# Performance work log

Measured on AMD Instinct MI355X. Metric: run time of the kernel, lower is better.

Reference implementation:

```python
import jax, jax.numpy as jnp
import numpy as np

DIM = 3456      # visual_dim
E = 1024        # embed_dim = dim_head*heads = 128*8
H = 8
D = E // H
LN_EPS = 1e-5


def _mlp(x, w1, b1, w2, b2):
    # nn.Sequential(Linear, GELU(exact), Linear)
    h = jax.nn.gelu(x @ w1.T + b1, approximate=False)
    return h @ w2.T + b2


def _ln(x, g, b):
    m = jnp.mean(x, axis=-1, keepdims=True)
    v = jnp.mean((x - m) ** 2, axis=-1, keepdims=True)
    return (x - m) * jax.lax.rsqrt(v + LN_EPS) * g + b


def setup_inputs() -> dict:
    key = jax.random.key(0)
    ks = jax.random.split(key, 24)
    std = 0.02
    d = {"x": jax.random.normal(ks[0], (5, 729, DIM), dtype=jnp.float32)}
    i = 1
    for name in ("q", "k", "v"):
        d[f"{name}_w1"] = std * jax.random.normal(ks[i], (E, DIM), dtype=jnp.float32); i += 1
        d[f"{name}_b1"] = jnp.zeros((E,), jnp.float32)
        d[f"{name}_w2"] = std * jax.random.normal(ks[i], (E, E), dtype=jnp.float32); i += 1
        d[f"{name}_b2"] = jnp.zeros((E,), jnp.float32)
        d[f"ln_{name}_g"] = jnp.ones((E,), jnp.float32)
        d[f"ln_{name}_b"] = jnp.zeros((E,), jnp.float32)
    d["in_proj_w"] = std * jax.random.normal(ks[i], (3 * E, E), dtype=jnp.float32); i += 1
    d["in_proj_b"] = jnp.zeros((3 * E,), jnp.float32)
    d["out_proj_w"] = std * jax.random.normal(ks[i], (E, E), dtype=jnp.float32); i += 1
    d["out_proj_b"] = jnp.zeros((E,), jnp.float32)
    d["to_out_w"] = std * jax.random.normal(ks[i], (DIM, E), dtype=jnp.float32)
    return d


def reference(x,
              q_w1, q_b1, q_w2, q_b2, ln_q_g, ln_q_b,
              k_w1, k_b1, k_w2, k_b2, ln_k_g, ln_k_b,
              v_w1, v_b1, v_w2, v_b2, ln_v_g, ln_v_b,
              in_proj_w, in_proj_b, out_proj_w, out_proj_b, to_out_w):
    t, hw, c = x.shape
    # spatial_temporal pattern: x_multi = x, no interpolation.
    # q/k/v: MLP -> LN -> permute(1,0,2) -> divide_feature -> flatten.
    # divide_feature is a pure permutation of tokens; all tokens end up in a
    # single (L, 1, E) attention, so full attention over the flattened
    # (hw, t) token order computes the identical result.
    q = _ln(_mlp(x, q_w1, q_b1, q_w2, q_b2), ln_q_g, ln_q_b)  # (t, hw, E)
    k = _ln(_mlp(x, k_w1, k_b1, k_w2, k_b2), ln_k_g, ln_k_b)
    v = _ln(_mlp(x, v_w1, v_b1, v_w2, v_b2), ln_v_g, ln_v_b)
    L = t * hw
    q = q.transpose(1, 0, 2).reshape(L, E)  # (hw*t, E), (h,w,t)-major order
    k = k.transpose(1, 0, 2).reshape(L, E)
    v = v.transpose(1, 0, 2).reshape(L, E)
    # nn.MultiheadAttention with packed in_proj
    qp = (q @ in_proj_w[:E].T + in_proj_b[:E]).reshape(L, H, D)
    kp = (k @ in_proj_w[E:2 * E].T + in_proj_b[E:2 * E]).reshape(L, H, D)
    vp = (v @ in_proj_w[2 * E:].T + in_proj_b[2 * E:]).reshape(L, H, D)
    scale = 1.0 / jnp.sqrt(jnp.asarray(D, q.dtype))
    scores = jnp.einsum('qhd,khd->hqk', qp, kp) * scale  # (H, L, L)
    attn = jax.nn.softmax(scores, axis=-1)
    o = jnp.einsum('hqk,khd->qhd', attn, vp).reshape(L, E)
    o = o @ out_proj_w.T + out_proj_b
    o = o.reshape(hw, t, E).transpose(1, 0, 2)  # (t, hw, E)
    out = o @ to_out_w.T                         # (t, hw, c)
    return x + out
```

## Files before the change

### kernel.cpp

```cpp
#include <hip/hip_runtime.h>
#include <hip/hip_bf16.h>

#define L_TOK 3645
#define MP    3712
#define DIMV  3456
#define EDIM  1024

typedef __attribute__((ext_vector_type(8))) short bf8;
typedef __attribute__((ext_vector_type(4))) short s4v;
typedef __attribute__((ext_vector_type(4))) float f4;

__device__ __forceinline__ short f2b(float f) {
  union { float f; unsigned u; } v; v.f = f;
  unsigned r = v.u + 0x7fffu + ((v.u >> 16) & 1u);
  return (short)(r >> 16);
}
__device__ __forceinline__ float b2f(short s) {
  union { unsigned u; float f; } v; v.u = ((unsigned)(unsigned short)s) << 16;
  return v.f;
}
__device__ __forceinline__ void gld16(const void* g, void* l) {
  __builtin_amdgcn_global_load_lds(
      (const __attribute__((address_space(1))) void*)(unsigned long long)g,
      (__attribute__((address_space(3))) void*)(unsigned)(unsigned long long)l,
      16, 0, 0);
}

__global__ __launch_bounds__(256) void k_cvt(const float* __restrict__ src,
                                             short* __restrict__ dst, int n4) {
  int i = blockIdx.x * 256 + threadIdx.x;
  if (i >= n4) return;
  float4 v = ((const float4*)src)[i];
  s4v o; o[0] = f2b(v.x); o[1] = f2b(v.y); o[2] = f2b(v.z); o[3] = f2b(v.w);
  ((s4v*)dst)[i] = o;
}
__global__ __launch_bounds__(256) void k_cvt_pad(const float* __restrict__ src,
                                                 short* __restrict__ dst, int n4src, int n4tot) {
  int i = blockIdx.x * 256 + threadIdx.x;
  if (i >= n4tot) return;
  s4v o; o[0] = 0; o[1] = 0; o[2] = 0; o[3] = 0;
  if (i < n4src) {
    float4 v = ((const float4*)src)[i];
    o[0] = f2b(v.x); o[1] = f2b(v.y); o[2] = f2b(v.z); o[3] = f2b(v.w);
  }
  ((s4v*)dst)[i] = o;
}

#define GM_GELU   0
#define GM_BIAS   1
#define GM_QSCALE 2
#define GM_RESID  3

template<int MODE>
__global__ __launch_bounds__(256)
void k_gemm(const short* __restrict__ A, long sA,
            const short* __restrict__ B, long sB,
            const float* __restrict__ bias0, const float* __restrict__ bias1,
            const float* __restrict__ bias2,
            void* __restrict__ Cout, long sC,
            int N, int K, const float* __restrict__ resid)
{
  __shared__ short As[3][128 * 32];
  __shared__ short Bs[3][128 * 32];
  const int tid  = threadIdx.x;
  const int z    = blockIdx.z;

  const int nwg  = gridDim.x * gridDim.y;
  const int orig = blockIdx.y * gridDim.x + blockIdx.x;
  const int qq   = nwg >> 3, rr = nwg & 7;
  const int xcd  = orig & 7, ofs = orig >> 3;
  const int swz  = (xcd < rr ? xcd * (qq + 1) : rr * (qq + 1) + (xcd - rr) * qq) + ofs;
  const int brow = (swz / gridDim.x) * 128;
  const int bcol = (swz % gridDim.x) * 128;

  const short* Ab = A + (long)z * sA;
  const short* Bb = B + (long)z * sB;
  const float* bias = (z == 0) ? bias0 : (z == 1 ? bias1 : bias2);

  const int wave = tid >> 6, lane = tid & 63;
  const int lg = lane >> 4, lc = lane & 15;
  const int m0 = (wave >> 1) * 64, n0 = (wave & 1) * 64;

  const int r0 = tid >> 2, seg = tid & 3;
  const int r1 = r0 + 64;
  const int so0 = (seg ^ ((r0 >> 1) & 3)) * 8;
  const int so1 = (seg ^ ((r1 >> 1) & 3)) * 8;
  const short* pA0 = Ab + (long)(brow + r0) * K + so0;
  const short* pA1 = Ab + (long)(brow + r1) * K + so1;
  const short* pB0 = Bb + (long)(bcol + r0) * K + so0;
  const short* pB1 = Bb + (long)(bcol + r1) * K + so1;

  f4 acc[4][4];
  f4 zero = {0.f, 0.f, 0.f, 0.f};
#pragma unroll
  for (int i = 0; i < 4; ++i)
#pragma unroll
    for (int j = 0; j < 4; ++j) acc[i][j] = zero;

  auto STAGE = [&](int buf) {
    gld16(pA0, &As[buf][tid * 8]);
    gld16(pA1, &As[buf][(tid + 256) * 8]);
    gld16(pB0, &Bs[buf][tid * 8]);
    gld16(pB1, &Bs[buf][(tid + 256) * 8]);
    pA0 += 32; pA1 += 32; pB0 += 32; pB1 += 32;
  };

  const int NT = K >> 5;
  STAGE(0);
  STAGE(1);

  for (int t = 0; t < NT; ++t) {
    const int buf = t % 3;
    if (t < NT - 1) { asm volatile("s_waitcnt vmcnt(4)" ::: "memory"); }
    else           { asm volatile("s_waitcnt vmcnt(0)" ::: "memory"); }
    __builtin_amdgcn_sched_barrier(0);
    __builtin_amdgcn_s_barrier();
    if (t + 2 < NT) STAGE((t + 2) % 3);

    const short* Al = &As[buf][0];
    const short* Bl = &Bs[buf][0];
    bf8 af[4], bfr[4];
#pragma unroll
    for (int mi = 0; mi < 4; ++mi) {
      int r = m0 + mi * 16 + lc;
      af[mi] = *(const bf8*)&Al[r * 32 + ((lg ^ ((r >> 1) & 3)) * 8)];
    }
#pragma unroll
    for (int ni = 0; ni < 4; ++ni) {
      int r = n0 + ni * 16 + lc;
      bfr[ni] = *(const bf8*)&Bl[r * 32 + ((lg ^ ((r >> 1) & 3)) * 8)];
    }
    __builtin_amdgcn_s_setprio(1);
#pragma unroll
    for (int mi = 0; mi < 4; ++mi)
#pragma unroll
      for (int ni = 0; ni < 4; ++ni)
        acc[mi][ni] = __builtin_amdgcn_mfma_f32_16x16x32_bf16(af[mi], bfr[ni], acc[mi][ni], 0, 0, 0);
    __builtin_amdgcn_s_setprio(0);
    __builtin_amdgcn_sched_barrier(0);
  }

  if (MODE == GM_RESID) {
    float* C = (float*)Cout;
#pragma unroll
    for (int ni = 0; ni < 4; ++ni) {
      int col = bcol + n0 + ni * 16 + lc;
#pragma unroll
      for (int mi = 0; mi < 4; ++mi)
#pragma unroll
        for (int r = 0; r < 4; ++r) {
          int row = brow + m0 + mi * 16 + lg * 4 + r;
          if (row < L_TOK)
            C[(long)row * N + col] = acc[mi][ni][r] + resid[(long)row * N + col];
        }
    }
  } else {
    short* C = (short*)Cout + (long)z * sC;
    const float alpha = (MODE == GM_QSCALE && z == 0) ? 0.08838834764831845f : 1.0f;
#pragma unroll
    for (int ni = 0; ni < 4; ++ni) {
      int col = bcol + n0 + ni * 16 + lc;
      float bv = bias[col];
#pragma unroll
      for (int mi = 0; mi < 4; ++mi)
#pragma unroll
        for (int r = 0; r < 4; ++r) {
          int row = brow + m0 + mi * 16 + lg * 4 + r;
          float v = acc[mi][ni][r] + bv;
          if (MODE == GM_GELU) v = 0.5f * v * (1.f + erff(v * 0.70710678118654752f));
          v *= alpha;
          C[(long)row * EDIM + col] = f2b(v);
        }
    }
  }
}

__global__ __launch_bounds__(256)
void k_ln(const short* __restrict__ A, short* __restrict__ Y,
          const float* __restrict__ g0, const float* __restrict__ g1, const float* __restrict__ g2,
          const float* __restrict__ b0, const float* __restrict__ b1, const float* __restrict__ b2)
{
  const int row = blockIdx.x, z = blockIdx.y;
  const float* g = (z == 0) ? g0 : (z == 1 ? g1 : g2);
  const float* b = (z == 0) ? b0 : (z == 1 ? b1 : b2);
  const short* a = A + ((long)z * MP + row) * EDIM;
  short* y = Y + ((long)z * MP + row) * EDIM;
  const int t = threadIdx.x;
  s4v v = *(const s4v*)&a[t * 4];
  float x0 = b2f(v[0]), x1 = b2f(v[1]), x2 = b2f(v[2]), x3 = b2f(v[3]);
  float s = x0 + x1 + x2 + x3;
  float q = x0 * x0 + x1 * x1 + x2 * x2 + x3 * x3;
#pragma unroll
  for (int off = 1; off < 64; off <<= 1) { s += __shfl_xor(s, off); q += __shfl_xor(q, off); }
  __shared__ float rs[4], rq[4];
  if ((t & 63) == 0) { rs[t >> 6] = s; rq[t >> 6] = q; }
  __syncthreads();
  s = rs[0] + rs[1] + rs[2] + rs[3];
  q = rq[0] + rq[1] + rq[2] + rq[3];
  float mean = s * (1.f / 1024.f);
  float var  = q * (1.f / 1024.f) - mean * mean;
  float rstd = rsqrtf(var + 1e-5f);
  s4v o;
#pragma unroll
  for (int j = 0; j < 4; ++j) {
    int col = t * 4 + j;
    o[j] = f2b((b2f(v[j]) - mean) * rstd * g[col] + b[col]);
  }
  *(s4v*)&y[t * 4] = o;
}

__global__ __launch_bounds__(256)
void k_vtrans(const short* __restrict__ vp, short* __restrict__ vpT)
{
  const int kb = blockIdx.x * 64, h = blockIdx.y;
  __shared__ short T[64 * 128];
  const int tid = threadIdx.x;
#pragma unroll
  for (int i = 0; i < 4; ++i) {
    int c = tid + 256 * i;
    int r = c >> 4, x = c & 15;
    bf8 val = *(const bf8*)&vp[(long)(kb + r) * EDIM + h * 128 + x * 8];
    *(bf8*)&T[r * 128 + ((x ^ (r & 7)) * 8)] = val;
  }
  __syncthreads();
#pragma unroll
  for (int i = 0; i < 4; ++i) {
    int c = tid + 256 * i;
    int dr = c >> 3, x = c & 7;
    short tmp[8];
#pragma unroll
    for (int e = 0; e < 8; ++e) {
      int kv = x * 8 + e;
      tmp[e] = T[kv * 128 + (((dr >> 3) ^ (kv & 7)) << 3) + (dr & 7)];
    }
    *(bf8*)&vpT[((long)h * 128 + dr) * MP + kb + x * 8] = *(bf8*)tmp;
  }
}

__global__ __launch_bounds__(256)
void k_attn(const short* __restrict__ qp, const short* __restrict__ kp,
            const short* __restrict__ vpT, short* __restrict__ o)
{
  const int bx = blockIdx.x;
  const int h = bx & 7, qb = (bx >> 3) * 64;
  const int tid = threadIdx.x, wave = tid >> 6, lane = tid & 63;
  const int lg = lane >> 4, lc = lane & 15;
  __shared__ short Ks[2][64 * 128];
  __shared__ short Vs[2][128 * 64];
  __shared__ short Ps[4][16 * 64];

  const int qrow = qb + wave * 16 + lc;
  bf8 qf[4];
#pragma unroll
  for (int d4 = 0; d4 < 4; ++d4)
    qf[d4] = *(const bf8*)&qp[(long)qrow * EDIM + h * 128 + d4 * 32 + lg * 8];

  f4 oacc[8];
  f4 zero = {0.f, 0.f, 0.f, 0.f};
#pragma unroll
  for (int dt = 0; dt < 8; ++dt) oacc[dt] = zero;
  float lsum = 0.f;

  auto STAGE = [&](short* ksb, short* vsb, int kb) {
#pragma unroll
    for (int i = 0; i < 4; ++i) {
      int c = tid + 256 * i; int r = c >> 4, x = c & 15;
      gld16(&kp[(long)(kb + r) * EDIM + h * 128 + (x ^ (r & 7)) * 8], &ksb[c * 8]);
    }
#pragma unroll
    for (int i = 0; i < 4; ++i) {
      int c = tid + 256 * i; int dr = c >> 3, x = c & 7;
      gld16(&vpT[((long)h * 128 + dr) * MP + kb + (x ^ (dr & 7)) * 8], &vsb[c * 8]);
    }
  };

  const int NTILE = (L_TOK + 63) / 64;
  STAGE(Ks[0], Vs[0], 0);

  for (int t = 0; t < NTILE; ++t) {
    const int kb = t * 64;
    const short* ksb = Ks[t & 1];
    const short* vsb = Vs[t & 1];
    __builtin_amdgcn_s_barrier();
    if (t + 1 < NTILE) {
      STAGE(Ks[(t + 1) & 1], Vs[(t + 1) & 1], kb + 64);
      asm volatile("s_waitcnt vmcnt(8)" ::: "memory");
    } else {
      asm volatile("s_waitcnt vmcnt(0)" ::: "memory");
    }
    __builtin_amdgcn_sched_barrier(0);
    __builtin_amdgcn_s_barrier();
    __builtin_amdgcn_sched_barrier(0);

#pragma unroll
    for (int s = 0; s < 4; ++s) {
      f4 sa = zero;
      const int krow = s * 16 + lc;
      bf8 kf[4];
#pragma unroll
      for (int d4 = 0; d4 < 4; ++d4)
        kf[d4] = *(const bf8*)&ksb[krow * 128 + (((d4 * 4 + lg) ^ (krow & 7)) * 8)];
      __builtin_amdgcn_s_setprio(1);
#pragma unroll
      for (int d4 = 0; d4 < 4; ++d4)
        sa = __builtin_amdgcn_mfma_f32_16x16x32_bf16(kf[d4], qf[d4], sa, 0, 0, 0);
      __builtin_amdgcn_s_setprio(0);
      const int kvb = kb + s * 16 + lg * 4;
      float p[4];
#pragma unroll
      for (int r = 0; r < 4; ++r) {
        float e = __expf(sa[r]);
        p[r] = (kvb + r < L_TOK) ? e : 0.f;
        lsum += p[r];
      }
      s4v pk; pk[0] = f2b(p[0]); pk[1] = f2b(p[1]); pk[2] = f2b(p[2]); pk[3] = f2b(p[3]);
      *(s4v*)&Ps[wave][lc * 64 + ((s * 16 + lg * 4) ^ ((lc & 7) << 3))] = pk;
    }
    bf8 pf0 = *(const bf8*)&Ps[wave][lc * 64 + ((lg * 8) ^ ((lc & 7) << 3))];
    bf8 pf1 = *(const bf8*)&Ps[wave][lc * 64 + ((32 + lg * 8) ^ ((lc & 7) << 3))];
#pragma unroll
    for (int dt = 0; dt < 8; ++dt) {
      const int vrow = dt * 16 + lc;
      bf8 vf0 = *(const bf8*)&vsb[vrow * 64 + ((lg ^ (vrow & 7)) * 8)];
      bf8 vf1 = *(const bf8*)&vsb[vrow * 64 + (((4 + lg) ^ (vrow & 7)) * 8)];
      __builtin_amdgcn_s_setprio(1);
      oacc[dt] = __builtin_amdgcn_mfma_f32_16x16x32_bf16(pf0, vf0, oacc[dt], 0, 0, 0);
      oacc[dt] = __builtin_amdgcn_mfma_f32_16x16x32_bf16(pf1, vf1, oacc[dt], 0, 0, 0);
      __builtin_amdgcn_s_setprio(0);
    }
    __builtin_amdgcn_sched_barrier(0);
  }

  lsum += __shfl_xor(lsum, 16);
  lsum += __shfl_xor(lsum, 32);
  float rinv[4];
#pragma unroll
  for (int r = 0; r < 4; ++r) rinv[r] = 1.f / __shfl(lsum, lg * 4 + r);
#pragma unroll
  for (int dt = 0; dt < 8; ++dt)
#pragma unroll
    for (int r = 0; r < 4; ++r) {
      int orow = qb + wave * 16 + lg * 4 + r;
      o[(long)orow * EDIM + h * 128 + dt * 16 + lc] = f2b(oacc[dt][r] * rinv[r]);
    }
}

extern "C" void kernel_launch(void* const* d_in, const int* in_sizes, int n_in,
                              void* d_out, int out_size, void* d_ws, size_t ws_size,
                              hipStream_t stream)
{
  const float* x   = (const float*)d_in[0];
  const float* ipb = (const float*)d_in[20];
  const float* opb = (const float*)d_in[22];

  char* ws = (char*)d_ws;
  short* regA = (short*)(ws + 0);
  short* regB = (short*)(ws + 25657344);
  short* w1b  = (short*)(ws + 48463872);
  short* w2b  = (short*)(ws + 69697536);
  short* wpb  = (short*)(ws + 75988992);
  short* wob  = (short*)(ws + 82280448);
  short* wtb  = (short*)(ws + 84377600);
  short* vpT  = (short*)(ws + 91455488);

  short* xb  = regA;
  short* h1  = regB;
  short* aln = regA;
  short* lnq = regB;
  short* proj = regA;
  short* ob  = regB;
  short* o2  = (short*)(ws + 25657344 + 7602176);

  k_cvt_pad<<<12528, 256, 0, stream>>>(x, xb, 3149280, 3207168);
  k_cvt<<<3456, 256, 0, stream>>>((const float*)d_in[1],  w1b,            884736);
  k_cvt<<<3456, 256, 0, stream>>>((const float*)d_in[7],  w1b + 3538944,  884736);
  k_cvt<<<3456, 256, 0, stream>>>((const float*)d_in[13], w1b + 7077888,  884736);
  k_cvt<<<1024, 256, 0, stream>>>((const float*)d_in[3],  w2b,            262144);
  k_cvt<<<1024, 256, 0, stream>>>((const float*)d_in[9],  w2b + 1048576,  262144);
  k_cvt<<<1024, 256, 0, stream>>>((const float*)d_in[15], w2b + 2097152,  262144);
  k_cvt<<<3072, 256, 0, stream>>>((const float*)d_in[19], wpb,            786432);
  k_cvt<<<1024, 256, 0, stream>>>((const float*)d_in[21], wob,            262144);
  k_cvt<<<3456, 256, 0, stream>>>((const float*)d_in[23], wtb,            884736);

  dim3 g3(8, 29, 3), g1(8, 29, 1);
  k_gemm<GM_GELU><<<g3, 256, 0, stream>>>(xb, 0, w1b, 3538944,
      (const float*)d_in[2], (const float*)d_in[8], (const float*)d_in[14],
      h1, (long)MP * EDIM, EDIM, DIMV, nullptr);
  k_gemm<GM_BIAS><<<g3, 256, 0, stream>>>(h1, (long)MP * EDIM, w2b, 1048576,
      (const float*)d_in[4], (const float*)d_in[10], (const float*)d_in[16],
      aln, (long)MP * EDIM, EDIM, EDIM, nullptr);
  dim3 gl(MP, 3);
  k_ln<<<gl, 256, 0, stream>>>(aln, lnq,
      (const float*)d_in[5], (const float*)d_in[11], (const float*)d_in[17],
      (const float*)d_in[6], (const float*)d_in[12], (const float*)d_in[18]);
  k_gemm<GM_QSCALE><<<g3, 256, 0, stream>>>(lnq, (long)MP * EDIM, wpb, 1048576,
      ipb, ipb + 1024, ipb + 2048,
      proj, (long)MP * EDIM, EDIM, EDIM, nullptr);
  dim3 gt(MP / 64, 8);
  k_vtrans<<<gt, 256, 0, stream>>>(proj + 2L * MP * EDIM, vpT);
  k_attn<<<(MP / 64) * 8, 256, 0, stream>>>(proj, proj + (long)MP * EDIM, vpT, ob);
  k_gemm<GM_BIAS><<<g1, 256, 0, stream>>>(ob, 0, wob, 0,
      opb, opb, opb, o2, 0, EDIM, EDIM, nullptr);
  dim3 g5(27, 29, 1);
  k_gemm<GM_RESID><<<g5, 256, 0, stream>>>(o2, 0, wtb, 0,
      nullptr, nullptr, nullptr, d_out, 0, DIMV, EDIM, x);
}
```

Baseline: 417.8 us.

## Double query rows per attention wave and shrink GEMM pipeline to two stages

The attention kernel now gives each wave 32 query rows (two 16-row groups) instead of 16, so every K/V tile staged in shared memory feeds twice the MFMA work, and the grid is halved. This cuts K/V global and LDS traffic per query but raises register pressure (two accumulator sets) and leaves fewer blocks to fill the GPU. Separately, the GEMM goes from triple to double buffering with a full vmcnt(0) wait each iteration. That frees LDS but exposes more load latency.

After: 421.6 us. Within noise of the previous version (+0.9%).

```diff
diff --git a/kernel.cpp b/kernel.cpp
--- a/kernel.cpp
+++ b/kernel.cpp
@@ -60,8 +60,8 @@
             void* __restrict__ Cout, long sC,
             int N, int K, const float* __restrict__ resid)
 {
-  __shared__ short As[3][128 * 32];
-  __shared__ short Bs[3][128 * 32];
+  __shared__ short As[2][128 * 32];
+  __shared__ short Bs[2][128 * 32];
   const int tid  = threadIdx.x;
   const int z    = blockIdx.z;
 
@@ -107,15 +107,13 @@
 
   const int NT = K >> 5;
   STAGE(0);
-  STAGE(1);
 
   for (int t = 0; t < NT; ++t) {
-    const int buf = t % 3;
-    if (t < NT - 1) { asm volatile("s_waitcnt vmcnt(4)" ::: "memory"); }
-    else           { asm volatile("s_waitcnt vmcnt(0)" ::: "memory"); }
+    const int buf = t & 1;
+    asm volatile("s_waitcnt vmcnt(0)" ::: "memory");
     __builtin_amdgcn_sched_barrier(0);
     __builtin_amdgcn_s_barrier();
-    if (t + 2 < NT) STAGE((t + 2) % 3);
+    if (t + 1 < NT) STAGE((t + 1) & 1);
 
     const short* Al = &As[buf][0];
     const short* Bl = &Bs[buf][0];
@@ -242,24 +240,28 @@
             const short* __restrict__ vpT, short* __restrict__ o)
 {
   const int bx = blockIdx.x;
-  const int h = bx & 7, qb = (bx >> 3) * 64;
+  const int h = bx & 7, qb = (bx >> 3) * 128;
   const int tid = threadIdx.x, wave = tid >> 6, lane = tid & 63;
   const int lg = lane >> 4, lc = lane & 15;
   __shared__ short Ks[2][64 * 128];
   __shared__ short Vs[2][128 * 64];
-  __shared__ short Ps[4][16 * 64];
-
-  const int qrow = qb + wave * 16 + lc;
-  bf8 qf[4];
-#pragma unroll
-  for (int d4 = 0; d4 < 4; ++d4)
-    qf[d4] = *(const bf8*)&qp[(long)qrow * EDIM + h * 128 + d4 * 32 + lg * 8];
-
-  f4 oacc[8];
+  __shared__ short Ps[4][32 * 64];
+
+  const int q0 = qb + wave * 32;
+  bf8 qf[2][4];
+#pragma unroll
+  for (int g = 0; g < 2; ++g)
+#pragma unroll
+    for (int d4 = 0; d4 < 4; ++d4)
+      qf[g][d4] = *(const bf8*)&qp[(long)(q0 + g * 16 + lc) * EDIM + h * 128 + d4 * 32 + lg * 8];
+
+  f4 oacc[2][8];
   f4 zero = {0.f, 0.f, 0.f, 0.f};
 #pragma unroll
-  for (int dt = 0; dt < 8; ++dt) oacc[dt] = zero;
-  float lsum = 0.f;
+  for (int g = 0; g < 2; ++g)
+#pragma unroll
+    for (int dt = 0; dt < 8; ++dt) oacc[g][dt] = zero;
+  float lsum0 = 0.f, lsum1 = 0.f;
 
   auto STAGE = [&](short* ksb, short* vsb, int kb) {
 #pragma unroll
@@ -294,55 +296,73 @@
 
 #pragma unroll
     for (int s = 0; s < 4; ++s) {
-      f4 sa = zero;
       const int krow = s * 16 + lc;
       bf8 kf[4];
 #pragma unroll
       for (int d4 = 0; d4 < 4; ++d4)
         kf[d4] = *(const bf8*)&ksb[krow * 128 + (((d4 * 4 + lg) ^ (krow & 7)) * 8)];
+      f4 sa0 = zero, sa1 = zero;
       __builtin_amdgcn_s_setprio(1);
 #pragma unroll
-      for (int d4 = 0; d4 < 4; ++d4)
-        sa = __builtin_amdgcn_mfma_f32_16x16x32_bf16(kf[d4], qf[d4], sa, 0, 0, 0);
+      for (int d4 = 0; d4 < 4; ++d4) {
+        sa0 = __builtin_amdgcn_mfma_f32_16x16x32_bf16(kf[d4], qf[0][d4], sa0, 0, 0, 0);
+        sa1 = __builtin_amdgcn_mfma_f32_16x16x32_bf16(kf[d4], qf[1][d4], sa1, 0, 0, 0);
+      }
       __builtin_amdgcn_s_setprio(0);
       const int kvb = kb + s * 16 + lg * 4;
-      float p[4];
-#pragma unroll
-      for (int r = 0; r < 4; ++r) {
-        float e = __expf(sa[r]);
-        p[r] = (kvb + r < L_TOK) ? e : 0.f;
-        lsum += p[r];
+#pragma unroll
+      for (int g = 0; g < 2; ++g) {
+        f4 sa = g ? sa1 : sa0;
+        float p[4];
+#pragma unroll
+        for (int r = 0; r < 4; ++r) {
+          float e = __expf(sa[r]);
+          p[r] = (kvb + r < L_TOK) ? e : 0.f;
+          if (g) lsum1 += p[r]; else lsum0 += p[r];
+        }
+        s4v pk; pk[0] = f2b(p[0]); pk[1] = f2b(p[1]); pk[2] = f2b(p[2]); pk[3] = f2b(p[3]);
+        *(s4v*)&Ps[wave][(g * 16 + lc) * 64 + ((s * 16 + lg * 4) ^ ((lc & 7) << 3))] = pk;
       }
-      s4v pk; pk[0] = f2b(p[0]); pk[1] = f2b(p[1]); pk[2] = f2b(p[2]); pk[3] = f2b(p[3]);
-      *(s4v*)&Ps[wave][lc * 64 + ((s * 16 + lg * 4) ^ ((lc & 7) << 3))] = pk;
-    }
-    bf8 pf0 = *(const bf8*)&Ps[wave][lc * 64 + ((lg * 8) ^ ((lc & 7) << 3))];
-    bf8 pf1 = *(const bf8*)&Ps[wave][lc * 64 + ((32 + lg * 8) ^ ((lc & 7) << 3))];
+    }
+    bf8 pf[2][2];
+#pragma unroll
+    for (int g = 0; g < 2; ++g) {
+      pf[g][0] = *(const bf8*)&Ps[wave][(g * 16 + lc) * 64 + ((lg * 8) ^ ((lc & 7) << 3))];
+      pf[g][1] = *(const bf8*)&Ps[wave][(g * 16 + lc) * 64 + ((32 + lg * 8) ^ ((lc & 7) << 3))];
+    }
 #pragma unroll
     for (int dt = 0; dt < 8; ++dt) {
       const int vrow = dt * 16 + lc;
       bf8 vf0 = *(const bf8*)&vsb[vrow * 64 + ((lg ^ (vrow & 7)) * 8)];
       bf8 vf1 = *(const bf8*)&vsb[vrow * 64 + (((4 + lg) ^ (vrow & 7)) * 8)];
       __builtin_amdgcn_s_setprio(1);
-      oacc[dt] = __builtin_amdgcn_mfma_f32_16x16x32_bf16(pf0, vf0, oacc[dt], 0, 0, 0);
-      oacc[dt] = __builtin_amdgcn_mfma_f32_16x16x32_bf16(pf1, vf1, oacc[dt], 0, 0, 0);
+      oacc[0][dt] = __builtin_amdgcn_mfma_f32_16x16x32_bf16(pf[0][0], vf0, oacc[0][dt], 0, 0, 0);
+      oacc[0][dt] = __builtin_amdgcn_mfma_f32_16x16x32_bf16(pf[0][1], vf1, oacc[0][dt], 0, 0, 0);
+      oacc[1][dt] = __builtin_amdgcn_mfma_f32_16x16x32_bf16(pf[1][0], vf0, oacc[1][dt], 0, 0, 0);
+      oacc[1][dt] = __builtin_amdgcn_mfma_f32_16x16x32_bf16(pf[1][1], vf1, oacc[1][dt], 0, 0, 0);
       __builtin_amdgcn_s_setprio(0);
     }
     __builtin_amdgcn_sched_barrier(0);
   }
 
-  lsum += __shfl_xor(lsum, 16);
-  lsum += __shfl_xor(lsum, 32);
-  float rinv[4];
-#pragma unroll
-  for (int r = 0; r < 4; ++r) rinv[r] = 1.f / __shfl(lsum, lg * 4 + r);
-#pragma unroll
-  for (int dt = 0; dt < 8; ++dt)
-#pragma unroll
-    for (int r = 0; r < 4; ++r) {
-      int orow = qb + wave * 16 + lg * 4 + r;
-      o[(long)orow * EDIM + h * 128 + dt * 16 + lc] = f2b(oacc[dt][r] * rinv[r]);
-    }
+  lsum0 += __shfl_xor(lsum0, 16);
+  lsum0 += __shfl_xor(lsum0, 32);
+  lsum1 += __shfl_xor(lsum1, 16);
+  lsum1 += __shfl_xor(lsum1, 32);
+#pragma unroll
+  for (int g = 0; g < 2; ++g) {
+    float ls = g ? lsum1 : lsum0;
+    float rinv[4];
+#pragma unroll
+    for (int r = 0; r < 4; ++r) rinv[r] = 1.f / __shfl(ls, lg * 4 + r);
+#pragma unroll
+    for (int dt = 0; dt < 8; ++dt)
+#pragma unroll
+      for (int r = 0; r < 4; ++r) {
+        int orow = q0 + g * 16 + lg * 4 + r;
+        o[(long)orow * EDIM + h * 128 + dt * 16 + lc] = f2b(oacc[g][dt][r] * rinv[r]);
+      }
+  }
 }
 
 extern "C" void kernel_launch(void* const* d_in, const int* in_sizes, int n_in,
@@ -398,7 +418,7 @@
       proj, (long)MP * EDIM, EDIM, EDIM, nullptr);
   dim3 gt(MP / 64, 8);
   k_vtrans<<<gt, 256, 0, stream>>>(proj + 2L * MP * EDIM, vpT);
-  k_attn<<<(MP / 64) * 8, 256, 0, stream>>>(proj, proj + (long)MP * EDIM, vpT, ob);
+  k_attn<<<(MP / 128) * 8, 256, 0, stream>>>(proj, proj + (long)MP * EDIM, vpT, ob);
   k_gemm<GM_BIAS><<<g1, 256, 0, stream>>>(ob, 0, wob, 0,
       opb, opb, opb, o2, 0, EDIM, EDIM, nullptr);
   dim3 g5(27, 29, 1);
```
